# Kernel tuning notes

Measured on AMD Instinct MI355X. Metric: run time of the kernel, lower is better.

Reference implementation:

```python
import jax, jax.numpy as jnp
import numpy as np

S = 256          # fine grid extent (active region within full_scale=4096)
SC = S // 2      # coarse grid extent after stride-2 downsample
N = 400_000      # active fine voxels
C_IN, M0, M1 = 3, 32, 64   # input features; unet_structure = [32, 64]
NCLASS = 20
EPS = 1e-4       # scn.BatchNormReLU default eps


def _build_nbr(keys_sorted, coords, s):
    """27-neighborhood index table for a sparse voxel set (hash via sorted keys)."""
    n = coords.shape[0]
    nbr = np.full((n, 27), -1, dtype=np.int32)
    x, y, z = coords[:, 0], coords[:, 1], coords[:, 2]
    k = 0
    for dx in (-1, 0, 1):
        for dy in (-1, 0, 1):
            for dz in (-1, 0, 1):
                nx, ny, nz = x + dx, y + dy, z + dz
                valid = (nx >= 0) & (nx < s) & (ny >= 0) & (ny < s) & (nz >= 0) & (nz < s)
                ck = (nx.astype(np.int64) * s + ny) * s + nz
                pos = np.clip(np.searchsorted(keys_sorted, ck), 0, n - 1)
                nbr[:, k] = np.where(valid & (keys_sorted[pos] == ck), pos, -1)
                k += 1
    return nbr


def setup_inputs() -> dict:
    rng = np.random.default_rng(0)
    keys = np.sort(rng.choice(S ** 3, size=N, replace=False).astype(np.int64))
    x = keys // (S * S); y = (keys // S) % S; z = keys % S
    coords = np.stack([x, y, z], 1)
    nbr_fine = _build_nbr(keys, coords, S)
    # stride-2 pooling structure
    ckeys = ((x // 2) * SC + (y // 2)) * SC + (z // 2)
    uk, parent_id = np.unique(ckeys, return_inverse=True)
    ccoords = np.stack([uk // (SC * SC), (uk // SC) % SC, uk % SC], 1)
    nbr_coarse = _build_nbr(uk, ccoords, SC)
    child_off = ((x & 1) * 4 + (y & 1) * 2 + (z & 1)).astype(np.int32)

    ks = jax.random.split(jax.random.key(0), 16)
    def w(k, shape, fan_in):
        return jax.random.normal(k, shape, jnp.float32) * (1.0 / np.sqrt(fan_in))
    return {
        "feats": jax.random.normal(ks[0], (N, C_IN), jnp.float32),
        "nbr_fine": jnp.asarray(nbr_fine),
        "nbr_coarse": jnp.asarray(nbr_coarse),
        "parent_id": jnp.asarray(parent_id.astype(np.int32)),
        "child_off": jnp.asarray(child_off),
        "W_sub": w(ks[1], (27, C_IN, M0), 27 * C_IN),
        "W_e0": w(ks[2], (27, M0, M0), 27 * M0),
        "g0": jnp.ones((M0,), jnp.float32), "b0": jnp.zeros((M0,), jnp.float32),
        "W_down": w(ks[3], (8, M0, M1), 8 * M0),
        "W_e1": w(ks[4], (27, M1, M1), 27 * M1),
        "g1": jnp.ones((M1,), jnp.float32), "b1": jnp.zeros((M1,), jnp.float32),
        "W_up": w(ks[5], (8, M1, M0), 8 * M1),
        "W_dec": w(ks[6], (27, 2 * M0, M0), 27 * 2 * M0),
        "g_out": jnp.ones((M0,), jnp.float32), "b_out": jnp.zeros((M0,), jnp.float32),
        "W_lin": w(ks[7], (M0, NCLASS), M0),
        "b_lin": jnp.zeros((NCLASS,), jnp.float32),
    }


def _subconv(feat, nbr, W):
    """Submanifold 3x3x3 conv: fixed loop over 27 kernel taps (gather+GEMM)."""
    out = jnp.zeros((feat.shape[0], W.shape[2]), feat.dtype)
    for k in range(27):
        idx = nbr[:, k]
        g = jnp.where(idx[:, None] >= 0, feat[jnp.clip(idx, 0)], 0.0)
        out = out + g @ W[k]
    return out


def _bnrelu(xv, g, b):
    mu = xv.mean(0)
    var = xv.var(0)
    return jax.nn.relu((xv - mu) * jax.lax.rsqrt(var + EPS) * g + b)


def reference(feats, nbr_fine, nbr_coarse, parent_id, child_off,
              W_sub, W_e0, g0, b0, W_down, W_e1, g1, b1, W_up, W_dec,
              g_out, b_out, W_lin, b_lin):
    M = nbr_coarse.shape[0]
    xv = _subconv(feats, nbr_fine, W_sub)                       # [N, M0]
    e0 = _bnrelu(_subconv(xv, nbr_fine, W_e0), g0, b0)          # encoder level 0
    # stride-2 sparse conv (scatter-add children into parents, per-offset weight)
    down = jax.ops.segment_sum(jnp.einsum('nc,ncd->nd', e0, W_down[child_off]),
                               parent_id, num_segments=M)        # [M, M1]
    e1 = _bnrelu(_subconv(down, nbr_coarse, W_e1), g1, b1)      # encoder level 1
    # stride-2 sparse deconv (gather parent, per-offset weight)
    up = jnp.einsum('nc,ncd->nd', e1[parent_id], W_up[child_off])  # [N, M0]
    dec = _subconv(jnp.concatenate([e0, up], 1), nbr_fine, W_dec)  # decoder join
    feature = _bnrelu(dec, g_out, b_out)                        # final BatchNormReLU
    y = feature @ W_lin + b_lin                                 # class head
    return (y, feature)
```

## Files before the change

kernel.cpp:

```cpp
#include <hip/hip_runtime.h>
#include <hip/hip_bf16.h>

#define BN_EPS 1e-4f

typedef __attribute__((ext_vector_type(8))) short short8;
typedef __attribute__((ext_vector_type(4))) float float4e;

__device__ __forceinline__ int rfl(int x) { return __builtin_amdgcn_readfirstlane(x); }

__device__ __forceinline__ float ldf(const __hip_bfloat16* p) { return __bfloat162float(*p); }
__device__ __forceinline__ void stf(__hip_bfloat16* p, float v) { *p = __float2bfloat16(v); }

__device__ __forceinline__ short bfbits(float x) {
    __hip_bfloat16 h = __float2bfloat16(x);
    short s;
    __builtin_memcpy(&s, &h, 2);
    return s;
}
__device__ __forceinline__ short8 cvt8(float4 a, float4 b) {
    short8 r;
    r[0] = bfbits(a.x); r[1] = bfbits(a.y); r[2] = bfbits(a.z); r[3] = bfbits(a.w);
    r[4] = bfbits(b.x); r[5] = bfbits(b.y); r[6] = bfbits(b.z); r[7] = bfbits(b.w);
    return r;
}

__global__ __launch_bounds__(256) void k_pack(const float* __restrict__ src,
                                              __hip_bfloat16* __restrict__ dst,
                                              int CIN, int COUT, int KT, int NT, int total) {
    int i = blockIdx.x * 256 + threadIdx.x;
    if (i >= total) return;
    int j = i & 7, lane = (i >> 3) & 63;
    int g = i >> 9;
    int nt = g % NT; g /= NT;
    int kt = g % KT; g /= KT;
    int t = g;
    int q = lane >> 4, c = lane & 15;
    dst[i] = __float2bfloat16(src[((size_t)t * CIN + kt * 32 + q * 8 + j) * COUT + nt * 16 + c]);
}

__global__ __launch_bounds__(256) void k_xv(const float* __restrict__ feats,
                                            const int* __restrict__ nbr,
                                            const float* __restrict__ W,
                                            __hip_bfloat16* __restrict__ out, int N) {
    int n = blockIdx.x * 256 + threadIdx.x;
    if (n >= N) return;
    float acc[32];
#pragma unroll
    for (int d = 0; d < 32; ++d) acc[d] = 0.f;
    const int* nb = nbr + (size_t)n * 27;
    for (int k = 0; k < 27; ++k) {
        int idx = nb[k];
        if (idx < 0) continue;
        float f0 = feats[(size_t)idx * 3 + 0];
        float f1 = feats[(size_t)idx * 3 + 1];
        float f2 = feats[(size_t)idx * 3 + 2];
        const float* w = W + k * 96;
#pragma unroll
        for (int d = 0; d < 32; ++d)
            acc[d] += f0 * w[d] + f1 * w[32 + d] + f2 * w[64 + d];
    }
    short8* o = (short8*)(out + (size_t)n * 32);
#pragma unroll
    for (int c = 0; c < 4; ++c) {
        short8 r;
#pragma unroll
        for (int j = 0; j < 8; ++j) r[j] = bfbits(acc[c * 8 + j]);
        o[c] = r;
    }
}

template <int CIN, int COUT, int MODE>
__global__ __launch_bounds__(256, 4) void k_conv(const void* __restrict__ inAv,
                                                 const void* __restrict__ inBv,
                                                 const int* __restrict__ nbr,
                                                 const __hip_bfloat16* __restrict__ Wp,
                                                 __hip_bfloat16* __restrict__ out,
                                                 int nrows,
                                                 float* __restrict__ ssum,
                                                 float* __restrict__ ssq) {
    constexpr int KT = CIN / 32;
    constexpr int NT = COUT / 16;
    static_assert(KT == 1 || KT == 2, "KT must be 1 or 2");
    __shared__ int sidx[4][432];
    const __hip_bfloat16* inAb = (const __hip_bfloat16*)inAv;
    const __hip_bfloat16* inBb = (const __hip_bfloat16*)inBv;
    const float* inAf = (const float*)inAv;
    const int tid = threadIdx.x;
    const int lane = tid & 63;
    const int wv = tid >> 6;
    const int m15 = lane & 15;
    const int q = lane >> 4;
    int* my = sidx[wv];
    const int b = blockIdx.x;
    const int bs = (b & 7) * (gridDim.x >> 3) + (b >> 3);
    const int w = bs * 4 + wv;
    const int nw = gridDim.x * 4;
    const int ntile = (nrows + 15) / 16;
    const int cq = ntile / nw, cr = ntile % nw;
    const int start = w * cq + (w < cr ? w : cr);
    const int tend = start + cq + (w < cr ? 1 : 0);
    float sS[NT], sQ[NT];
#pragma unroll
    for (int nt = 0; nt < NT; ++nt) { sS[nt] = 0.f; sQ[nt] = 0.f; }

    const short8 z8 = (short8)(short)0;

    for (int tile = start; tile < tend; ++tile) {
        const int row0 = rfl(tile) * 16;
        int nr = nrows - row0;
        nr = nr > 16 ? 16 : nr;
        const int* src = nbr + (size_t)row0 * 27;
        const int tot = nr * 27;
        for (int t = lane; t < 432; t += 64) my[t] = (t < tot) ? src[t] : -1;
        float4e acc[NT];
#pragma unroll
        for (int nt = 0; nt < NT; ++nt) acc[nt] = (float4e)0.f;

        short8 sA0 = z8, sA1 = z8, sB0 = z8, sB1 = z8, sC0 = z8, sC1 = z8;
        float4 fA0{}, fA1{}, fA2{}, fA3{};
        float4 fB0{}, fB1{}, fB2{}, fB3{};
        float4 fC0{}, fC1{}, fC2{}, fC3{};

        auto load_g = [&](int ir, short8& s0, short8& s1,
                          float4& f0, float4& f1, float4& f2, float4& f3) {
            size_t id = (size_t)(ir < 0 ? 0 : ir);
            if constexpr (MODE == 0) {
                s0 = *(const short8*)(inAb + id * CIN + q * 8);
                if constexpr (KT == 2)
                    s1 = *(const short8*)(inAb + id * CIN + 32 + q * 8);
            } else if constexpr (MODE == 2) {
                s0 = *(const short8*)(inAb + id * 32 + q * 8);
                s1 = *(const short8*)(inBb + id * 32 + q * 8);
            } else {
                const float* bb = inAf + id * 64 + q * 8;
                f0 = *(const float4*)(bb);
                f1 = *(const float4*)(bb + 4);
                f2 = *(const float4*)(bb + 32);
                f3 = *(const float4*)(bb + 36);
            }
        };

        int irA = my[m15 * 27 + 0];
        int irB = my[m15 * 27 + 1];
        int irC = my[m15 * 27 + 2];
        int mA = rfl((int)(__ballot(irA >= 0) & 0xffff));
        int mB = rfl((int)(__ballot(irB >= 0) & 0xffff));
        if (mA) load_g(irA, sA0, sA1, fA0, fA1, fA2, fA3);
        if (mB) load_g(irB, sB0, sB1, fB0, fB1, fB2, fB3);
        for (int k = 0; k < 27; ++k) {
            int mC = rfl((int)(__ballot(irC >= 0) & 0xffff));
            int irD = -1;
            if (k + 3 < 27) irD = my[m15 * 27 + (k + 3)];
            if (mC) load_g(irC, sC0, sC1, fC0, fC1, fC2, fC3);
            if (mA) {
                short8 a0, a1;
                if constexpr (MODE == 1) {
                    a0 = cvt8(fA0, fA1);
                    a1 = cvt8(fA2, fA3);
                } else {
                    a0 = sA0;
                    a1 = sA1;
                }
                a0 = (irA >= 0) ? a0 : z8;
                if constexpr (KT == 2) a1 = (irA >= 0) ? a1 : z8;
                const short8* bp = (const short8*)Wp + (size_t)k * KT * NT * 64 + lane;
#pragma unroll
                for (int nt = 0; nt < NT; ++nt) {
                    acc[nt] = __builtin_amdgcn_mfma_f32_16x16x32_bf16(a0, bp[nt * 64], acc[nt], 0, 0, 0);
                    if constexpr (KT == 2)
                        acc[nt] = __builtin_amdgcn_mfma_f32_16x16x32_bf16(a1, bp[(NT + nt) * 64], acc[nt], 0, 0, 0);
                }
            }
            mA = mB; mB = mC;
            irA = irB; irB = irC; irC = irD;
            if constexpr (MODE == 1) {
                fA0 = fB0; fA1 = fB1; fA2 = fB2; fA3 = fB3;
                fB0 = fC0; fB1 = fC1; fB2 = fC2; fB3 = fC3;
            } else {
                sA0 = sB0; sB0 = sC0;
                if constexpr (KT == 2) { sA1 = sB1; sB1 = sC1; }
            }
        }
#pragma unroll
        for (int nt = 0; nt < NT; ++nt) {
#pragma unroll
            for (int r = 0; r < 4; ++r) {
                int rowg = row0 + q * 4 + r;
                if (rowg < nrows) {
                    float v = acc[nt][r];
                    stf(out + (size_t)rowg * COUT + nt * 16 + m15, v);
                    sS[nt] += v;
                    sQ[nt] += v * v;
                }
            }
        }
    }
#pragma unroll
    for (int nt = 0; nt < NT; ++nt) {
        float v = sS[nt], w2 = sQ[nt];
        v += __shfl_xor(v, 16); v += __shfl_xor(v, 32);
        w2 += __shfl_xor(w2, 16); w2 += __shfl_xor(w2, 32);
        if (lane < 16) {
            atomicAdd(&ssum[nt * 16 + lane], v);
            atomicAdd(&ssq[nt * 16 + lane], w2);
        }
    }
}

__global__ void k_fin(const float* __restrict__ ssum, const float* __restrict__ ssq,
                      const float* __restrict__ g, const float* __restrict__ b,
                      float* __restrict__ scale, float* __restrict__ shift,
                      int C, float invN) {
    int c = blockIdx.x * blockDim.x + threadIdx.x;
    if (c >= C) return;
    float mu = ssum[c] * invN;
    float var = fmaxf(ssq[c] * invN - mu * mu, 0.f);
    float s = g[c] * rsqrtf(var + BN_EPS);
    scale[c] = s;
    shift[c] = b[c] - mu * s;
}

__global__ __launch_bounds__(256) void k_down(__hip_bfloat16* __restrict__ e0,
                                              const int* __restrict__ parent,
                                              const int* __restrict__ child,
                                              const float* __restrict__ Wd,
                                              const float* __restrict__ sc,
                                              const float* __restrict__ sh,
                                              float* __restrict__ down, int N) {
    const int lane = threadIdx.x & 63;
    int wid = blockIdx.x * 4 + (threadIdx.x >> 6);
    int nw = gridDim.x * 4;
    for (int row = wid; row < N; row += nw) {
        int urow = rfl(row);
        float v = 0.f;
        if (lane < 32) {
            float r = ldf(e0 + (size_t)urow * 32 + lane);
            v = fmaxf(fmaf(r, sc[lane], sh[lane]), 0.f);
            stf(e0 + (size_t)urow * 32 + lane, v);
        }
        int par = rfl(parent[urow]);
        int off = rfl(child[urow]);
        float acc = 0.f;
        const float* wb = Wd + (size_t)off * 2048 + lane;
#pragma unroll
        for (int c = 0; c < 32; ++c)
            acc = fmaf(__shfl(v, c), wb[c * 64], acc);
        atomicAdd(&down[(size_t)par * 64 + lane], acc);
    }
}

__global__ __launch_bounds__(256) void k_up(const __hip_bfloat16* __restrict__ e1raw,
                                            const int* __restrict__ parent,
                                            const int* __restrict__ child,
                                            const float* __restrict__ Wu,
                                            const float* __restrict__ sc,
                                            const float* __restrict__ sh,
                                            __hip_bfloat16* __restrict__ up, int N) {
    const int lane = threadIdx.x & 63;
    int wid = blockIdx.x * 4 + (threadIdx.x >> 6);
    int nw = gridDim.x * 4;
    for (int row = wid; row < N; row += nw) {
        int urow = rfl(row);
        int par = rfl(parent[urow]);
        int off = rfl(child[urow]);
        float e = ldf(e1raw + (size_t)par * 64 + lane);
        float v = fmaxf(fmaf(e, sc[lane], sh[lane]), 0.f);
        int d = lane & 31, hi = lane >> 5;
        float acc = 0.f;
        const float* wb = Wu + (size_t)off * 2048 + (size_t)hi * 1024 + d;
#pragma unroll
        for (int c = 0; c < 32; ++c)
            acc = fmaf(__shfl(v, hi * 32 + c), wb[c * 32], acc);
        acc += __shfl_xor(acc, 32);
        if (hi == 0) stf(up + (size_t)urow * 32 + d, acc);
    }
}

__global__ __launch_bounds__(256) void k_out(const __hip_bfloat16* __restrict__ dec,
                                             const float* __restrict__ sc,
                                             const float* __restrict__ sh,
                                             const float* __restrict__ Wl,
                                             const float* __restrict__ bl,
                                             float* __restrict__ y,
                                             float* __restrict__ feat, int N) {
    int n = blockIdx.x * 256 + threadIdx.x;
    if (n >= N) return;
    float f[32];
    const __hip_bfloat162* p = (const __hip_bfloat162*)(dec + (size_t)n * 32);
#pragma unroll
    for (int j = 0; j < 16; ++j) {
        float2 t = __bfloat1622float2(p[j]);
        f[2 * j + 0] = fmaxf(fmaf(t.x, sc[2 * j + 0], sh[2 * j + 0]), 0.f);
        f[2 * j + 1] = fmaxf(fmaf(t.y, sc[2 * j + 1], sh[2 * j + 1]), 0.f);
    }
    float4* fo = (float4*)(feat + (size_t)n * 32);
#pragma unroll
    for (int j = 0; j < 8; ++j)
        fo[j] = make_float4(f[4 * j], f[4 * j + 1], f[4 * j + 2], f[4 * j + 3]);
    float acc[20];
#pragma unroll
    for (int qq = 0; qq < 20; ++qq) acc[qq] = bl[qq];
#pragma unroll
    for (int c = 0; c < 32; ++c) {
        float fc = f[c];
#pragma unroll
        for (int qq = 0; qq < 20; ++qq) acc[qq] = fmaf(fc, Wl[c * 20 + qq], acc[qq]);
    }
    float4* yo = (float4*)(y + (size_t)n * 20);
#pragma unroll
    for (int j = 0; j < 5; ++j)
        yo[j] = make_float4(acc[4 * j], acc[4 * j + 1], acc[4 * j + 2], acc[4 * j + 3]);
}

extern "C" void kernel_launch(void* const* d_in, const int* in_sizes, int n_in,
                              void* d_out, int out_size, void* d_ws, size_t ws_size,
                              hipStream_t stream) {
    const float* feats = (const float*)d_in[0];
    const int* nbr_f   = (const int*)d_in[1];
    const int* nbr_c   = (const int*)d_in[2];
    const int* parent  = (const int*)d_in[3];
    const int* child   = (const int*)d_in[4];
    const float* W_sub = (const float*)d_in[5];
    const float* W_e0  = (const float*)d_in[6];
    const float* g0    = (const float*)d_in[7];
    const float* b0    = (const float*)d_in[8];
    const float* W_dn  = (const float*)d_in[9];
    const float* W_e1  = (const float*)d_in[10];
    const float* g1    = (const float*)d_in[11];
    const float* b1    = (const float*)d_in[12];
    const float* W_up  = (const float*)d_in[13];
    const float* W_dec = (const float*)d_in[14];
    const float* g_o   = (const float*)d_in[15];
    const float* b_o   = (const float*)d_in[16];
    const float* W_lin = (const float*)d_in[17];
    const float* b_lin = (const float*)d_in[18];

    const int N = in_sizes[0] / 3;
    const int M = in_sizes[2] / 27;

    float* wsf = (float*)d_ws;
    size_t R = (size_t)M * 64;
    if ((size_t)N * 32 > R) R = (size_t)N * 32;
    __hip_bfloat16* xvb = (__hip_bfloat16*)wsf;
    float* down = wsf;
    __hip_bfloat16* up     = (__hip_bfloat16*)wsf;
    __hip_bfloat16* decraw = (__hip_bfloat16*)(wsf + (size_t)N * 16);
    float* stats = wsf + R;

    __hip_bfloat16* e0    = (__hip_bfloat16*)d_out;
    __hip_bfloat16* e1raw = (__hip_bfloat16*)((float*)d_out + (size_t)N * 16);
    __hip_bfloat16* Wp0   = (__hip_bfloat16*)((float*)d_out + (size_t)N * 16 + (size_t)M * 32);
    const int T0 = 27 * 1 * 2 * 512;
    const int T1 = 27 * 2 * 4 * 512;
    const int T2 = 27 * 2 * 2 * 512;
    __hip_bfloat16* Wp1 = Wp0 + T0;
    __hip_bfloat16* Wp2 = Wp1 + T1;
    float* y    = (float*)d_out;
    float* feat = y + (size_t)N * 20;

    const int nblk = (N + 255) / 256;
    const int G = 2048;

    hipMemsetAsync(stats, 0, 256 * sizeof(float), stream);
    k_pack<<<(T0 + 255) / 256, 256, 0, stream>>>(W_e0, Wp0, 32, 32, 1, 2, T0);
    k_pack<<<(T1 + 255) / 256, 256, 0, stream>>>(W_e1, Wp1, 64, 64, 2, 4, T1);
    k_pack<<<(T2 + 255) / 256, 256, 0, stream>>>(W_dec, Wp2, 64, 32, 2, 2, T2);

    k_xv<<<nblk, 256, 0, stream>>>(feats, nbr_f, W_sub, xvb, N);
    k_conv<32, 32, 0><<<G, 256, 0, stream>>>(xvb, nullptr, nbr_f, Wp0, e0, N,
                                             stats + 0, stats + 32);
    hipMemsetAsync(down, 0, (size_t)M * 64 * sizeof(float), stream);
    k_fin<<<1, 64, 0, stream>>>(stats + 0, stats + 32, g0, b0,
                                stats + 256, stats + 288, 32, 1.f / (float)N);
    k_down<<<G, 256, 0, stream>>>(e0, parent, child, W_dn,
                                  stats + 256, stats + 288, down, N);
    k_conv<64, 64, 1><<<G, 256, 0, stream>>>(down, nullptr, nbr_c, Wp1, e1raw, M,
                                             stats + 64, stats + 128);
    k_fin<<<1, 64, 0, stream>>>(stats + 64, stats + 128, g1, b1,
                                stats + 320, stats + 384, 64, 1.f / (float)M);
    k_up<<<G, 256, 0, stream>>>(e1raw, parent, child, W_up,
                                stats + 320, stats + 384, up, N);
    k_conv<64, 32, 2><<<G, 256, 0, stream>>>(e0, up, nbr_f, Wp2, decraw, N,
                                             stats + 192, stats + 224);
    k_fin<<<1, 64, 0, stream>>>(stats + 192, stats + 224, g_o, b_o,
                                stats + 448, stats + 480, 32, 1.f / (float)N);
    k_out<<<nblk, 256, 0, stream>>>(decraw, stats + 448, stats + 480, W_lin, b_lin,
                                    y, feat, N);
}
```

Before: 1.632 ms.

## Convert coarse conv input to split bf16 halves and interleave tiles per XCD

```diff
diff --git a/kernel.cpp b/kernel.cpp
--- a/kernel.cpp
+++ b/kernel.cpp
@@ -67,6 +67,20 @@
         for (int j = 0; j < 8; ++j) r[j] = bfbits(acc[c * 8 + j]);
         o[c] = r;
     }
+}
+
+__global__ __launch_bounds__(256) void k_cvt2(const float* __restrict__ src,
+                                              __hip_bfloat16* __restrict__ lo,
+                                              __hip_bfloat16* __restrict__ hi, int M) {
+    int i = blockIdx.x * 256 + threadIdx.x;
+    if (i >= M * 8) return;
+    int row = i >> 3;
+    int c8 = i & 7;
+    const float4* p = (const float4*)(src + (size_t)row * 64 + c8 * 8);
+    float4 a = p[0], b = p[1];
+    __hip_bfloat16* dst = (c8 < 4) ? (lo + (size_t)row * 32 + c8 * 8)
+                                   : (hi + (size_t)row * 32 + (c8 - 4) * 8);
+    *(short8*)dst = cvt8(a, b);
 }
 
 template <int CIN, int COUT, int MODE>
@@ -92,20 +106,19 @@
     const int q = lane >> 4;
     int* my = sidx[wv];
     const int b = blockIdx.x;
-    const int bs = (b & 7) * (gridDim.x >> 3) + (b >> 3);
-    const int w = bs * 4 + wv;
-    const int nw = gridDim.x * 4;
+    const int xcd = b & 7;
+    const int wpx = (gridDim.x >> 3) * 4;
+    const int lw = (b >> 3) * 4 + wv;
     const int ntile = (nrows + 15) / 16;
-    const int cq = ntile / nw, cr = ntile % nw;
-    const int start = w * cq + (w < cr ? w : cr);
-    const int tend = start + cq + (w < cr ? 1 : 0);
+    const int s0 = (int)(((long long)xcd * ntile) >> 3);
+    const int s1 = (int)(((long long)(xcd + 1) * ntile) >> 3);
     float sS[NT], sQ[NT];
 #pragma unroll
     for (int nt = 0; nt < NT; ++nt) { sS[nt] = 0.f; sQ[nt] = 0.f; }
 
     const short8 z8 = (short8)(short)0;
 
-    for (int tile = start; tile < tend; ++tile) {
+    for (int tile = s0 + lw; tile < s1; tile += wpx) {
         const int row0 = rfl(tile) * 16;
         int nr = nrows - row0;
         nr = nr > 16 ? 16 : nr;
@@ -121,16 +134,16 @@
         float4 fB0{}, fB1{}, fB2{}, fB3{};
         float4 fC0{}, fC1{}, fC2{}, fC3{};
 
-        auto load_g = [&](int ir, short8& s0, short8& s1,
+        auto load_g = [&](int ir, short8& s0_, short8& s1_,
                           float4& f0, float4& f1, float4& f2, float4& f3) {
             size_t id = (size_t)(ir < 0 ? 0 : ir);
             if constexpr (MODE == 0) {
-                s0 = *(const short8*)(inAb + id * CIN + q * 8);
+                s0_ = *(const short8*)(inAb + id * CIN + q * 8);
                 if constexpr (KT == 2)
-                    s1 = *(const short8*)(inAb + id * CIN + 32 + q * 8);
+                    s1_ = *(const short8*)(inAb + id * CIN + 32 + q * 8);
             } else if constexpr (MODE == 2) {
-                s0 = *(const short8*)(inAb + id * 32 + q * 8);
-                s1 = *(const short8*)(inBb + id * 32 + q * 8);
+                s0_ = *(const short8*)(inAb + id * 32 + q * 8);
+                s1_ = *(const short8*)(inBb + id * 32 + q * 8);
             } else {
                 const float* bb = inAf + id * 64 + q * 8;
                 f0 = *(const float4*)(bb);
@@ -374,8 +387,20 @@
                                 stats + 256, stats + 288, 32, 1.f / (float)N);
     k_down<<<G, 256, 0, stream>>>(e0, parent, child, W_dn,
                                   stats + 256, stats + 288, down, N);
-    k_conv<64, 64, 1><<<G, 256, 0, stream>>>(down, nullptr, nbr_c, Wp1, e1raw, M,
-                                             stats + 64, stats + 128);
+    {
+        size_t base = (R + 512) * sizeof(float);
+        size_t needb = base + (size_t)M * 64 * sizeof(__hip_bfloat16);
+        if (ws_size >= needb) {
+            __hip_bfloat16* dlo = (__hip_bfloat16*)((char*)d_ws + base);
+            __hip_bfloat16* dhi = dlo + (size_t)M * 32;
+            k_cvt2<<<((M * 8) + 255) / 256, 256, 0, stream>>>(down, dlo, dhi, M);
+            k_conv<64, 64, 2><<<G, 256, 0, stream>>>(dlo, dhi, nbr_c, Wp1, e1raw, M,
+                                                     stats + 64, stats + 128);
+        } else {
+            k_conv<64, 64, 1><<<G, 256, 0, stream>>>(down, nullptr, nbr_c, Wp1, e1raw, M,
+                                                     stats + 64, stats + 128);
+        }
+    }
     k_fin<<<1, 64, 0, stream>>>(stats + 64, stats + 128, g1, b1,
                                 stats + 320, stats + 384, 64, 1.f / (float)M);
     k_up<<<G, 256, 0, stream>>>(e1raw, parent, child, W_up,
```

New measurement: 2.571 ms. +57.5%, slower.
